# Performance work log

Measured on AMD Instinct MI355X. Metric: run time of the kernel, lower is better.

The kernel has to match this reference:

```python
import jax, jax.numpy as jnp
import numpy as np

B, T, D = 4, 2048, 768
E, F, K = 8, 4 * 768, 2


def setup_inputs() -> dict:
    key = jax.random.key(0)
    ks = jax.random.split(key, 5)
    s = 0.02
    return {
        "x": jax.random.normal(ks[0], (B, T, D), dtype=jnp.float32),
        "Wg": jax.random.normal(ks[1], (D, E), dtype=jnp.float32) * s,
        "bg": jnp.zeros((E,), dtype=jnp.float32),
        "W1": jax.random.normal(ks[2], (E, D, F), dtype=jnp.float32) * s,
        "b1": jnp.zeros((E, F), dtype=jnp.float32),
        "W2": jax.random.normal(ks[3], (E, F, D), dtype=jnp.float32) * s,
        "b2": jnp.zeros((E, D), dtype=jnp.float32),
    }


def reference(x, Wg, bg, W1, b1, W2, b2):
    b, t, d = x.shape
    x_flat = x.reshape(-1, d)                      # [N, D]
    n = x_flat.shape[0]

    # Router: softmax over expert logits, take top-2
    gates = jax.nn.softmax(x_flat @ Wg + bg, axis=-1)   # [N, E]
    topk_g, topk_i = jax.lax.top_k(gates, K)            # [N, K]

    # Combine weights: zero for non-selected experts -> math identical to
    # masked dispatch in the torch loop (out = sum_k gate_k * expert_{idx_k}(x))
    combine = jnp.zeros((n, W1.shape[0]), dtype=gates.dtype)
    combine = combine.at[jnp.arange(n)[:, None], topk_i].add(topk_g)  # [N, E]

    # Per-expert MLP applied densely, then weighted combine (zero weights
    # kill non-selected experts' contributions)
    h = jnp.einsum('nd,edf->enf', x_flat, W1) + b1[:, None, :]  # [E, N, F]
    h = jax.nn.gelu(h, approximate=False)                        # torch nn.GELU = exact
    y = jnp.einsum('enf,efd->end', h, W2) + b2[:, None, :]       # [E, N, D]
    out = jnp.einsum('ne,end->nd', combine, y)                   # [N, D]
    return out.reshape(b, t, d)
```

## Files before the change

### kernel.cpp

```cpp
#include <hip/hip_runtime.h>
#include <hip/hip_bf16.h>


#define N_TOK 8192
#define D_DIM 768
#define E_EXP 8
#define F_DIM 3072
#define CAP   8192
#define NT_MAX 136

typedef __attribute__((ext_vector_type(8))) short s8v;
typedef __attribute__((ext_vector_type(4))) float f4v;
typedef unsigned short u16;
typedef unsigned int   u32;
typedef unsigned long long u64;

static __device__ __forceinline__ u16 f2bf(float f) {
    u32 u = __float_as_uint(f);
    return (u16)((u + 0x7fffu + ((u >> 16) & 1u)) >> 16);
}
static __device__ __forceinline__ float bf2f(u16 v) {
    return __uint_as_float((u32)v << 16);
}
static __device__ __forceinline__ u32 cvt_pk_bf16(float lo, float hi) {
    u32 r;
    asm("v_cvt_pk_bf16_f32 %0, %1, %2" : "=v"(r) : "v"(lo), "v"(hi));
    return r;
}
static __device__ __forceinline__ float gelu_fast(float v) {
    const float av = fabsf(v);
    const float z  = av * 0.70710678118654752440f;
    const float t  = __builtin_amdgcn_rcpf(fmaf(0.3275911f, z, 1.0f));
    const float w  = __builtin_amdgcn_exp2f(-z * z * 1.4426950408889634f);
    float p = fmaf(1.061405429f, t, -1.453152027f);
    p = fmaf(p, t,  1.421413741f);
    p = fmaf(p, t, -0.284496736f);
    p = fmaf(p, t,  0.254829592f);
    p = p * t;
    const float E = 1.0f - p * w;
    return 0.5f * (v + av * E);
}
static __device__ __forceinline__ void gld_lds16(const u16* g, u16* l) {
    __builtin_amdgcn_global_load_lds(
        (const __attribute__((address_space(1))) void*)g,
        (__attribute__((address_space(3))) void*)l, 16, 0, 0);
}
template<int N> static __device__ __forceinline__ void wait_vmcnt() {
    asm volatile("s_waitcnt vmcnt(%0)" :: "n"(N) : "memory");
}
static __device__ __forceinline__ void bar_fenced() {
    asm volatile("s_barrier" ::: "memory");
}

__device__ __forceinline__ void pack_w_body(
    const float* __restrict__ src, u16* __restrict__ dst,
    int rt, int kc64, int e, int K1, int M2, int KC2, int TR, int ntm)
{
    __shared__ float ls[64][132];
    const float* se = src + (size_t)e * K1 * M2;
    const int tid = threadIdx.x;

    const int kr = tid >> 2, mq = tid & 3;
    const float* srow = se + (size_t)(kc64 * 64 + kr) * M2 + rt * 128 + mq * 32;
    #pragma unroll
    for (int it = 0; it < 8; ++it)
        *(float4*)&ls[kr][mq * 32 + it * 4] = *(const float4*)(srow + it * 4);
    __syncthreads();

    u16* dt_ = dst + ((size_t)(e * ntm + (rt * 128) / TR) * KC2 + kc64 * 2)
                     * ((size_t)TR * 32)
                   + (size_t)((rt * 128) % TR) * 32;
    const int rr = tid >> 1, hf = tid & 1;
    u16* dc = dt_ + (size_t)hf * TR * 32;
    const int row = ((rt * 128) % TR) + rr;
    #pragma unroll
    for (int j = 0; j < 4; ++j) {
        union { s8v v; u16 u[8]; } o;
        #pragma unroll
        for (int jj = 0; jj < 8; ++jj)
            o.u[jj] = f2bf(ls[hf * 32 + j * 8 + jj][rr]);
        *(s8v*)&dc[(size_t)rr * 32 + ((j ^ ((row >> 1) & 3)) * 8)] = o.v;
    }
}

__global__ __launch_bounds__(256) void prep_kernel(
    const float* __restrict__ x, const float* __restrict__ Wg,
    const float* __restrict__ bg, const float* __restrict__ W1,
    const float* __restrict__ W2, u32* __restrict__ rec_idx,
    float2* __restrict__ rec_g, u16* __restrict__ w1g,
    u16* __restrict__ w2g, int* __restrict__ counts)
{
    const int bid = blockIdx.x;
    if (bid == 0 && threadIdx.x < E_EXP) counts[threadIdx.x] = 0;

    if (bid < 2048) {
        const int wave = threadIdx.x >> 6;
        const int lane = threadIdx.x & 63;
        const int t = bid * 4 + wave;

        float acc[8];
        #pragma unroll
        for (int e = 0; e < 8; ++e) acc[e] = 0.f;

        const float* xrow = x + (size_t)t * D_DIM + lane * 12;
        #pragma unroll
        for (int i = 0; i < 3; ++i) {
            float4 xv = *(const float4*)(xrow + i * 4);
            float xs[4] = {xv.x, xv.y, xv.z, xv.w};
            #pragma unroll
            for (int j = 0; j < 4; ++j) {
                const int d = lane * 12 + i * 4 + j;
                const float4 w0 = *(const float4*)(Wg + (size_t)d * 8);
                const float4 w1 = *(const float4*)(Wg + (size_t)d * 8 + 4);
                acc[0] += xs[j] * w0.x;  acc[1] += xs[j] * w0.y;
                acc[2] += xs[j] * w0.z;  acc[3] += xs[j] * w0.w;
                acc[4] += xs[j] * w1.x;  acc[5] += xs[j] * w1.y;
                acc[6] += xs[j] * w1.z;  acc[7] += xs[j] * w1.w;
            }
        }
        #pragma unroll
        for (int e = 0; e < 8; ++e) {
            float v = acc[e];
            #pragma unroll
            for (int off = 32; off > 0; off >>= 1) v += __shfl_xor(v, off, 64);
            acc[e] = v + bg[e];
        }
        if (lane == 0) {
            float mx = acc[0];
            #pragma unroll
            for (int e = 1; e < 8; ++e) mx = fmaxf(mx, acc[e]);
            float p[8], s = 0.f;
            #pragma unroll
            for (int e = 0; e < 8; ++e) { p[e] = expf(acc[e] - mx); s += p[e]; }
            const float inv = 1.f / s;
            #pragma unroll
            for (int e = 0; e < 8; ++e) p[e] *= inv;

            int i0 = 0; float g0 = p[0];
            #pragma unroll
            for (int e = 1; e < 8; ++e) if (p[e] > g0) { g0 = p[e]; i0 = e; }
            int i1 = -1; float g1 = -1.f;
            #pragma unroll
            for (int e = 0; e < 8; ++e) if (e != i0 && p[e] > g1) { g1 = p[e]; i1 = e; }

            rec_idx[t] = (u32)i0 | ((u32)i1 << 4);
            rec_g[t] = make_float2(g0, g1);
        }
    } else if (bid < 4352) {
        const int id = bid - 2048;
        const int e = id / 288, rem = id - e * 288;
        const int rt = rem / 12, kc = rem - rt * 12;
        pack_w_body(W1, w1g, rt, kc, e, D_DIM, F_DIM, 24, 256, 12);
    } else {
        const int id = bid - 4352;
        const int e = id / 288, rem = id - e * 288;
        const int rt = rem / 48, kc = rem - rt * 48;
        pack_w_body(W2, w2g, rt, kc, e, F_DIM, D_DIM, 96, 256, 3);
    }
}

__global__ __launch_bounds__(256) void moe_scatter(
    const u32* __restrict__ rec_idx, const float2* __restrict__ rec_g,
    int* __restrict__ counts, int* __restrict__ tokbuf,
    float* __restrict__ gatebuf)
{
    const int t = blockIdx.x * 256 + threadIdx.x;
    const int lane = threadIdx.x & 63;
    const u32 pk = rec_idx[t];
    const int i0 = pk & 15, i1 = (pk >> 4) & 15;
    const float2 g = rec_g[t];
    const u64 lmask = ((u64)1 << lane) - 1;

    #pragma unroll
    for (int e = 0; e < 8; ++e) {
        const u64 m0 = __ballot(i0 == e);
        const u64 m1 = __ballot(i1 == e);
        const int c0 = __popcll(m0);
        const int total = c0 + __popcll(m1);
        if (total > 0) {
            int base = 0;
            if (lane == 0) base = atomicAdd(&counts[e], total);
            base = __shfl(base, 0, 64);
            if (i0 == e) {
                const int p = base + __popcll(m0 & lmask);
                tokbuf[(size_t)e * CAP + p] = 2 * t;
                gatebuf[(size_t)e * CAP + p] = g.x;
            }
            if (i1 == e) {
                const int p = base + c0 + __popcll(m1 & lmask);
                tokbuf[(size_t)e * CAP + p] = 2 * t + 1;
                gatebuf[(size_t)e * CAP + p] = g.y;
            }
        }
    }
}

__global__ void scan_kernel(const int* __restrict__ counts,
                            int* __restrict__ te, int* __restrict__ tb,
                            int* __restrict__ ntile) {
    if (threadIdx.x == 0) {
        int nt = 0;
        for (int e = 0; e < E_EXP; ++e)
            for (int k = 0; k * 128 < counts[e]; ++k) {
                te[nt] = e; tb[nt] = k * 128; ++nt;
            }
        *ntile = nt;
    }
}

__global__ __launch_bounds__(256) void pack_x(
    const float* __restrict__ x, const int* __restrict__ counts,
    const int* __restrict__ te, const int* __restrict__ tb,
    const int* __restrict__ ntile, const int* __restrict__ tokbuf,
    u16* __restrict__ xg)
{
    const int bx = blockIdx.x, kc = blockIdx.y;
    if (bx >= *ntile) return;
    const int e = te[bx], base = tb[bx], cnt = counts[e];
    const int tid = threadIdx.x;
    const int r = tid >> 1, hf = tid & 1;
    int ent = base + r; if (ent >= cnt) ent = cnt - 1;
    const int tok = tokbuf[(size_t)e * CAP + ent] >> 1;
    const float* xr = x + (size_t)tok * D_DIM + kc * 64 + hf * 32;
    u16* xt = xg + ((size_t)bx * 24 + kc * 2 + hf) * 4096;
    #pragma unroll
    for (int j = 0; j < 4; ++j) {
        float4 a = *(const float4*)(xr + j * 8);
        float4 b = *(const float4*)(xr + j * 8 + 4);
        union { s8v v; u16 u[8]; } o;
        o.u[0] = f2bf(a.x); o.u[1] = f2bf(a.y); o.u[2] = f2bf(a.z); o.u[3] = f2bf(a.w);
        o.u[4] = f2bf(b.x); o.u[5] = f2bf(b.y); o.u[6] = f2bf(b.z); o.u[7] = f2bf(b.w);
        *(s8v*)&xt[(size_t)r * 32 + ((j ^ ((r >> 1) & 3)) * 8)] = o.v;
    }
}

#define G_STAGE(S, SBUF) do {                                                 \
    const int S__ = (S) < NS_ ? (S) : NS_ - 1;                                \
    const u16* An_ = Ab + (size_t)S__ * 8192 + w * 2048 + lane * 8;           \
    const u16* Bn_ = Bb + (size_t)S__ * 4096 + w * 1024 + lane * 8;           \
    u16* Ad_ = &Als[SBUF][w * 2048];                                          \
    u16* Bd_ = &Bls[SBUF][w * 1024];                                          \
    gld_lds16(An_,        Ad_);                                               \
    gld_lds16(An_ +  512, Ad_ +  512);                                        \
    gld_lds16(An_ + 1024, Ad_ + 1024);                                        \
    gld_lds16(An_ + 1536, Ad_ + 1536);                                        \
    gld_lds16(Bn_,        Bd_);                                               \
    gld_lds16(Bn_ +  512, Bd_ +  512);                                        \
} while (0)

#define G_STEP(S, BUF, B2) do {                                               \
    wait_vmcnt<6>();                                                          \
    bar_fenced();                                                             \
    G_STAGE((S) + 2, B2);                                                     \
    s8v af[8], bf[4];                                                         \
    _Pragma("unroll")                                                         \
    for (int mi = 0; mi < 8; ++mi)                                            \
        af[mi] = *(const s8v*)&Als[BUF][(wm*128 + mi*16 + ln)*32 + colU];     \
    _Pragma("unroll")                                                         \
    for (int ni = 0; ni < 4; ++ni)                                            \
        bf[ni] = *(const s8v*)&Bls[BUF][(wn*64 + ni*16 + ln)*32 + colU];      \
    __builtin_amdgcn_s_setprio(1);                                            \
    _Pragma("unroll")                                                         \
    for (int mi = 0; mi < 8; ++mi)                                            \
        _Pragma("unroll")                                                     \
        for (int ni = 0; ni < 4; ++ni)                                        \
            acc[mi][ni] = __builtin_amdgcn_mfma_f32_16x16x32_bf16(            \
                af[mi], bf[ni], acc[mi][ni], 0, 0, 0);                        \
    __builtin_amdgcn_s_setprio(0);                                            \
} while (0)

__global__ __launch_bounds__(256, 2) void s1_gemm(
    const u16* __restrict__ xg, const u16* __restrict__ w1g,
    const float* __restrict__ b1, const int* __restrict__ te,
    const int* __restrict__ ntile, u16* __restrict__ hg)
{
    __shared__ __align__(16) u16 Als[3][8192];
    __shared__ __align__(16) u16 Bls[3][4096];
    const int bx = blockIdx.x, by = blockIdx.y;
    if (bx >= *ntile) return;
    const int e = te[bx];
    const int NS_ = 24;

    const int tid  = threadIdx.x;
    const int w    = tid >> 6;
    const int lane = tid & 63;
    const int wm   = w & 1, wn = w >> 1;
    const int q    = lane >> 4, ln = lane & 15;
    const int colU = (q ^ ((ln >> 1) & 3)) * 8;

    const u16* Ab = w1g + (size_t)(e * 12 + by) * 24 * 8192;
    const u16* Bb = xg  + (size_t)bx * 24 * 4096;

    f4v acc[8][4];
    #pragma unroll
    for (int mi = 0; mi < 8; ++mi)
        #pragma unroll
        for (int ni = 0; ni < 4; ++ni) acc[mi][ni] = (f4v){0.f,0.f,0.f,0.f};

    G_STAGE(0, 0);
    G_STAGE(1, 1);

    #pragma unroll 1
    for (int k = 0; k < 24; k += 3) {
        G_STEP(k,     0, 2);
        G_STEP(k + 1, 1, 0);
        G_STEP(k + 2, 2, 1);
    }
    wait_vmcnt<0>();

    const float* b1e = b1 + (size_t)e * F_DIM + by * 256;
    #pragma unroll
    for (int mi = 0; mi < 8; ++mi) {
        const int floc = wm * 128 + mi * 16 + q * 4;
        const int kc2  = by * 8 + (floc >> 5);
        const int cg   = (floc >> 3) & 3;
        const float4 bv = *(const float4*)&b1e[floc];
        #pragma unroll
        for (int ni = 0; ni < 4; ++ni) {
            const int rr = wn * 64 + ni * 16 + ln;
            uint2 pk;
            pk.x = cvt_pk_bf16(gelu_fast(acc[mi][ni][0] + bv.x),
                               gelu_fast(acc[mi][ni][1] + bv.y));
            pk.y = cvt_pk_bf16(gelu_fast(acc[mi][ni][2] + bv.z),
                               gelu_fast(acc[mi][ni][3] + bv.w));
            *(uint2*)&hg[((size_t)bx * 96 + kc2) * 4096 +
                         (size_t)rr * 32 + ((cg ^ ((rr >> 1) & 3)) * 8) +
                         (q & 1) * 4] = pk;
        }
    }
}

__global__ __launch_bounds__(256, 2) void s2_gemm(
    const u16* __restrict__ hg, const u16* __restrict__ w2g,
    const int* __restrict__ counts, const int* __restrict__ te,
    const int* __restrict__ tb, const int* __restrict__ ntile,
    const int* __restrict__ tokbuf, const float* __restrict__ gatebuf,
    u16* __restrict__ y)
{
    __shared__ __align__(16) u16 Als[3][8192];
    __shared__ __align__(16) u16 Bls[3][4096];
    __shared__ int   sts[128];
    __shared__ float sg[128];
    const int bx = blockIdx.x, by = blockIdx.y;
    if (bx >= *ntile) return;
    const int e = te[bx], base = tb[bx], cnt = counts[e];
    const int NS_ = 96;

    const int tid  = threadIdx.x;
    const int w    = tid >> 6;
    const int lane = tid & 63;
    const int wm   = w & 1, wn = w >> 1;
    const int q    = lane >> 4, ln = lane & 15;
    const int colU = (q ^ ((ln >> 1) & 3)) * 8;

    if (tid < 128) {
        const int ent = base + tid;
        const bool v = ent < cnt;
        sts[tid] = v ? tokbuf[(size_t)e * CAP + ent] : -1;
        sg[tid]  = v ? gatebuf[(size_t)e * CAP + ent] : 0.f;
    }
    asm volatile("s_waitcnt vmcnt(0) lgkmcnt(0)" ::: "memory");
    bar_fenced();

    const u16* Ab = w2g + (size_t)(e * 3 + by) * 96 * 8192;
    const u16* Bb = hg  + (size_t)bx * 96 * 4096;

    f4v acc[8][4];
    #pragma unroll
    for (int mi = 0; mi < 8; ++mi)
        #pragma unroll
        for (int ni = 0; ni < 4; ++ni) acc[mi][ni] = (f4v){0.f,0.f,0.f,0.f};

    G_STAGE(0, 0);
    G_STAGE(1, 1);

    #pragma unroll 1
    for (int k = 0; k < 96; k += 3) {
        G_STEP(k,     0, 2);
        G_STEP(k + 1, 1, 0);
        G_STEP(k + 2, 2, 1);
    }
    wait_vmcnt<0>();

    #pragma unroll
    for (int ni = 0; ni < 4; ++ni) {
        const int rr = wn * 64 + ni * 16 + ln;
        const int ts = sts[rr];
        if (ts >= 0) {
            const float g = sg[rr];
            u16* yr = y + (size_t)ts * D_DIM + by * 256 + wm * 128 + q * 4;
            #pragma unroll
            for (int mi = 0; mi < 8; ++mi) {
                uint2 pk;
                pk.x = cvt_pk_bf16(g * acc[mi][ni][0], g * acc[mi][ni][1]);
                pk.y = cvt_pk_bf16(g * acc[mi][ni][2], g * acc[mi][ni][3]);
                *(uint2*)&yr[mi * 16] = pk;
            }
        }
    }
}

__global__ __launch_bounds__(256) void combine_kernel(
    const u16* __restrict__ y, const u32* __restrict__ rec_idx,
    const float2* __restrict__ rec_g, const float* __restrict__ b2,
    float* __restrict__ out)
{
    const int gid = blockIdx.x * 256 + threadIdx.x;
    const int t = gid / 192;
    const int c = (gid - t * 192) * 4;
    const u32 pk = rec_idx[t];
    const int i0 = pk & 15, i1 = (pk >> 4) & 15;
    const float2 g = rec_g[t];
    union { uint2 p; u16 u[4]; } a, b;
    a.p = *(const uint2*)&y[(size_t)(2 * t) * D_DIM + c];
    b.p = *(const uint2*)&y[(size_t)(2 * t + 1) * D_DIM + c];
    const float4 ba = *(const float4*)&b2[(size_t)i0 * D_DIM + c];
    const float4 bb = *(const float4*)&b2[(size_t)i1 * D_DIM + c];
    float4 o;
    o.x = g.x * ba.x + g.y * bb.x + bf2f(a.u[0]) + bf2f(b.u[0]);
    o.y = g.x * ba.y + g.y * bb.y + bf2f(a.u[1]) + bf2f(b.u[1]);
    o.z = g.x * ba.z + g.y * bb.z + bf2f(a.u[2]) + bf2f(b.u[2]);
    o.w = g.x * ba.w + g.y * bb.w + bf2f(a.u[3]) + bf2f(b.u[3]);
    *(float4*)&out[(size_t)t * D_DIM + c] = o;
}

extern "C" void kernel_launch(void* const* d_in, const int* in_sizes, int n_in,
                              void* d_out, int out_size, void* d_ws, size_t ws_size,
                              hipStream_t stream) {
    const float* x  = (const float*)d_in[0];
    const float* Wg = (const float*)d_in[1];
    const float* bg = (const float*)d_in[2];
    const float* W1 = (const float*)d_in[3];
    const float* b1 = (const float*)d_in[4];
    const float* W2 = (const float*)d_in[5];
    const float* b2 = (const float*)d_in[6];
    float* out = (float*)d_out;

    char* ws = (char*)d_ws;
    size_t off = 0;
    u16* xg  = (u16*)(ws + off); off += (size_t)NT_MAX * 24 * 4096 * sizeof(u16);
    u16* w1g = (u16*)(ws + off); off += (size_t)E_EXP * F_DIM * D_DIM * sizeof(u16);
    u16* w2g = (u16*)(ws + off); off += (size_t)E_EXP * D_DIM * F_DIM * sizeof(u16);
    u16* hg  = (u16*)(ws + off); off += (size_t)NT_MAX * 96 * 4096 * sizeof(u16);
    u16* y   = (u16*)(ws + off); off += (size_t)2 * N_TOK * D_DIM * sizeof(u16);
    int* tokbuf = (int*)(ws + off);      off += (size_t)E_EXP * CAP * sizeof(int);
    float* gatebuf = (float*)(ws + off); off += (size_t)E_EXP * CAP * sizeof(float);
    u32* rec_idx = (u32*)(ws + off);     off += (size_t)N_TOK * sizeof(u32);
    float2* rec_g = (float2*)(ws + off); off += (size_t)N_TOK * sizeof(float2);
    int* counts = (int*)(ws + off);      off += 64;
    int* te     = (int*)(ws + off);      off += NT_MAX * sizeof(int);
    int* tb     = (int*)(ws + off);      off += NT_MAX * sizeof(int);
    int* ntile  = (int*)(ws + off);      off += 64;

    prep_kernel<<<6656, 256, 0, stream>>>(x, Wg, bg, W1, W2, rec_idx, rec_g,
                                          w1g, w2g, counts);
    moe_scatter<<<N_TOK / 256, 256, 0, stream>>>(rec_idx, rec_g, counts, tokbuf, gatebuf);
    scan_kernel<<<1, 64, 0, stream>>>(counts, te, tb, ntile);
    pack_x<<<dim3(NT_MAX, 12), 256, 0, stream>>>(x, counts, te, tb, ntile, tokbuf, xg);

    s1_gemm<<<dim3(NT_MAX, 12), 256, 0, stream>>>(xg, w1g, b1, te, ntile, hg);
    s2_gemm<<<dim3(NT_MAX, 3), 256, 0, stream>>>(hg, w2g, counts, te, tb, ntile,
                                                 tokbuf, gatebuf, y);
    combine_kernel<<<(N_TOK * 192) / 256, 256, 0, stream>>>(y, rec_idx, rec_g, b2, out);
}
```

Before: 511.1 us.

## Enlarge expert GEMM token tiles to 256 and switch to 32x32x16 MFMA

Doubles the token tile per expert from 128 to 256 rows in both expert GEMMs and pack_x. Each wave now computes a 128x128 sub-tile with 32x32x16 bf16 MFMA instructions instead of 16x16x32, which raises arithmetic intensity per LDS read and per weight load. The cost is more LDS per block and fewer resident blocks (launch bounds drop to 1 block per SM). Padding waste also grows for experts whose token counts are not multiples of 256, and the grid shrinks, which may under-fill the GPU.

```diff
diff --git a/kernel.cpp b/kernel.cpp
--- a/kernel.cpp
+++ b/kernel.cpp
@@ -7,10 +7,10 @@
 #define E_EXP 8
 #define F_DIM 3072
 #define CAP   8192
-#define NT_MAX 136
-
-typedef __attribute__((ext_vector_type(8))) short s8v;
-typedef __attribute__((ext_vector_type(4))) float f4v;
+#define NT2_MAX 72
+
+typedef __attribute__((ext_vector_type(8)))  short s8v;
+typedef __attribute__((ext_vector_type(16))) float f16v;
 typedef unsigned short u16;
 typedef unsigned int   u32;
 typedef unsigned long long u64;
@@ -201,8 +201,8 @@
     if (threadIdx.x == 0) {
         int nt = 0;
         for (int e = 0; e < E_EXP; ++e)
-            for (int k = 0; k * 128 < counts[e]; ++k) {
-                te[nt] = e; tb[nt] = k * 128; ++nt;
+            for (int k = 0; k * 256 < counts[e]; ++k) {
+                te[nt] = e; tb[nt] = k * 256; ++nt;
             }
         *ntile = nt;
     }
@@ -214,15 +214,17 @@
     const int* __restrict__ ntile, const int* __restrict__ tokbuf,
     u16* __restrict__ xg)
 {
-    const int bx = blockIdx.x, kc = blockIdx.y;
+    const int bx2 = blockIdx.x, kc = blockIdx.y;
+    const int bx = bx2 >> 1, rh = bx2 & 1;
     if (bx >= *ntile) return;
     const int e = te[bx], base = tb[bx], cnt = counts[e];
     const int tid = threadIdx.x;
     const int r = tid >> 1, hf = tid & 1;
-    int ent = base + r; if (ent >= cnt) ent = cnt - 1;
+    const int R = rh * 128 + r;
+    int ent = base + R; if (ent >= cnt) ent = cnt - 1;
     const int tok = tokbuf[(size_t)e * CAP + ent] >> 1;
     const float* xr = x + (size_t)tok * D_DIM + kc * 64 + hf * 32;
-    u16* xt = xg + ((size_t)bx * 24 + kc * 2 + hf) * 4096;
+    u16* xt = xg + ((size_t)bx * 24 + kc * 2 + hf) * 8192;
     #pragma unroll
     for (int j = 0; j < 4; ++j) {
         float4 a = *(const float4*)(xr + j * 8);
@@ -230,52 +232,58 @@
         union { s8v v; u16 u[8]; } o;
         o.u[0] = f2bf(a.x); o.u[1] = f2bf(a.y); o.u[2] = f2bf(a.z); o.u[3] = f2bf(a.w);
         o.u[4] = f2bf(b.x); o.u[5] = f2bf(b.y); o.u[6] = f2bf(b.z); o.u[7] = f2bf(b.w);
-        *(s8v*)&xt[(size_t)r * 32 + ((j ^ ((r >> 1) & 3)) * 8)] = o.v;
+        *(s8v*)&xt[(size_t)R * 32 + ((j ^ ((R >> 1) & 3)) * 8)] = o.v;
     }
 }
 
 #define G_STAGE(S, SBUF) do {                                                 \
     const int S__ = (S) < NS_ ? (S) : NS_ - 1;                                \
     const u16* An_ = Ab + (size_t)S__ * 8192 + w * 2048 + lane * 8;           \
-    const u16* Bn_ = Bb + (size_t)S__ * 4096 + w * 1024 + lane * 8;           \
+    const u16* Bn_ = Bb + (size_t)S__ * 8192 + w * 2048 + lane * 8;           \
     u16* Ad_ = &Als[SBUF][w * 2048];                                          \
-    u16* Bd_ = &Bls[SBUF][w * 1024];                                          \
+    u16* Bd_ = &Bls[SBUF][w * 2048];                                          \
     gld_lds16(An_,        Ad_);                                               \
     gld_lds16(An_ +  512, Ad_ +  512);                                        \
     gld_lds16(An_ + 1024, Ad_ + 1024);                                        \
     gld_lds16(An_ + 1536, Ad_ + 1536);                                        \
     gld_lds16(Bn_,        Bd_);                                               \
     gld_lds16(Bn_ +  512, Bd_ +  512);                                        \
+    gld_lds16(Bn_ + 1024, Bd_ + 1024);                                        \
+    gld_lds16(Bn_ + 1536, Bd_ + 1536);                                        \
 } while (0)
 
 #define G_STEP(S, BUF, B2) do {                                               \
-    wait_vmcnt<6>();                                                          \
+    wait_vmcnt<8>();                                                          \
     bar_fenced();                                                             \
     G_STAGE((S) + 2, B2);                                                     \
-    s8v af[8], bf[4];                                                         \
     _Pragma("unroll")                                                         \
-    for (int mi = 0; mi < 8; ++mi)                                            \
-        af[mi] = *(const s8v*)&Als[BUF][(wm*128 + mi*16 + ln)*32 + colU];     \
-    _Pragma("unroll")                                                         \
-    for (int ni = 0; ni < 4; ++ni)                                            \
-        bf[ni] = *(const s8v*)&Bls[BUF][(wn*64 + ni*16 + ln)*32 + colU];      \
-    __builtin_amdgcn_s_setprio(1);                                            \
-    _Pragma("unroll")                                                         \
-    for (int mi = 0; mi < 8; ++mi)                                            \
+    for (int kk = 0; kk < 2; ++kk) {                                          \
+        const int cswz = ((kk * 2 + hi) ^ ((r32 >> 1) & 3)) * 8;              \
+        s8v af[4], bf[4];                                                     \
         _Pragma("unroll")                                                     \
-        for (int ni = 0; ni < 4; ++ni)                                        \
-            acc[mi][ni] = __builtin_amdgcn_mfma_f32_16x16x32_bf16(            \
-                af[mi], bf[ni], acc[mi][ni], 0, 0, 0);                        \
-    __builtin_amdgcn_s_setprio(0);                                            \
+        for (int mt = 0; mt < 4; ++mt)                                        \
+            af[mt] = *(const s8v*)&Als[BUF][(wm*128 + mt*32 + r32)*32 + cswz];\
+        _Pragma("unroll")                                                     \
+        for (int nt = 0; nt < 4; ++nt)                                        \
+            bf[nt] = *(const s8v*)&Bls[BUF][(wn*128 + nt*32 + r32)*32 + cswz];\
+        __builtin_amdgcn_s_setprio(1);                                        \
+        _Pragma("unroll")                                                     \
+        for (int mt = 0; mt < 4; ++mt)                                        \
+            _Pragma("unroll")                                                 \
+            for (int nt = 0; nt < 4; ++nt)                                    \
+                acc[mt][nt] = __builtin_amdgcn_mfma_f32_32x32x16_bf16(        \
+                    af[mt], bf[nt], acc[mt][nt], 0, 0, 0);                    \
+        __builtin_amdgcn_s_setprio(0);                                        \
+    }                                                                         \
 } while (0)
 
-__global__ __launch_bounds__(256, 2) void s1_gemm(
+__global__ __launch_bounds__(256, 1) void s1_gemm(
     const u16* __restrict__ xg, const u16* __restrict__ w1g,
     const float* __restrict__ b1, const int* __restrict__ te,
     const int* __restrict__ ntile, u16* __restrict__ hg)
 {
     __shared__ __align__(16) u16 Als[3][8192];
-    __shared__ __align__(16) u16 Bls[3][4096];
+    __shared__ __align__(16) u16 Bls[3][8192];
     const int bx = blockIdx.x, by = blockIdx.y;
     if (bx >= *ntile) return;
     const int e = te[bx];
@@ -285,17 +293,18 @@
     const int w    = tid >> 6;
     const int lane = tid & 63;
     const int wm   = w & 1, wn = w >> 1;
-    const int q    = lane >> 4, ln = lane & 15;
-    const int colU = (q ^ ((ln >> 1) & 3)) * 8;
+    const int r32  = lane & 31, hi = lane >> 5;
 
     const u16* Ab = w1g + (size_t)(e * 12 + by) * 24 * 8192;
-    const u16* Bb = xg  + (size_t)bx * 24 * 4096;
-
-    f4v acc[8][4];
-    #pragma unroll
-    for (int mi = 0; mi < 8; ++mi)
-        #pragma unroll
-        for (int ni = 0; ni < 4; ++ni) acc[mi][ni] = (f4v){0.f,0.f,0.f,0.f};
+    const u16* Bb = xg  + (size_t)bx * 24 * 8192;
+
+    f16v acc[4][4];
+    #pragma unroll
+    for (int mt = 0; mt < 4; ++mt)
+        #pragma unroll
+        for (int nt = 0; nt < 4; ++nt)
+            #pragma unroll
+            for (int ee = 0; ee < 16; ++ee) acc[mt][nt][ee] = 0.f;
 
     G_STAGE(0, 0);
     G_STAGE(1, 1);
@@ -310,27 +319,30 @@
 
     const float* b1e = b1 + (size_t)e * F_DIM + by * 256;
     #pragma unroll
-    for (int mi = 0; mi < 8; ++mi) {
-        const int floc = wm * 128 + mi * 16 + q * 4;
-        const int kc2  = by * 8 + (floc >> 5);
-        const int cg   = (floc >> 3) & 3;
-        const float4 bv = *(const float4*)&b1e[floc];
-        #pragma unroll
-        for (int ni = 0; ni < 4; ++ni) {
-            const int rr = wn * 64 + ni * 16 + ln;
-            uint2 pk;
-            pk.x = cvt_pk_bf16(gelu_fast(acc[mi][ni][0] + bv.x),
-                               gelu_fast(acc[mi][ni][1] + bv.y));
-            pk.y = cvt_pk_bf16(gelu_fast(acc[mi][ni][2] + bv.z),
-                               gelu_fast(acc[mi][ni][3] + bv.w));
-            *(uint2*)&hg[((size_t)bx * 96 + kc2) * 4096 +
-                         (size_t)rr * 32 + ((cg ^ ((rr >> 1) & 3)) * 8) +
-                         (q & 1) * 4] = pk;
-        }
-    }
-}
-
-__global__ __launch_bounds__(256, 2) void s2_gemm(
+    for (int mt = 0; mt < 4; ++mt) {
+        const int kc2 = by * 8 + wm * 4 + mt;
+        u16* hc = hg + ((size_t)bx * 96 + kc2) * 8192;
+        #pragma unroll
+        for (int rq = 0; rq < 4; ++rq) {
+            const int floc = wm * 128 + mt * 32 + rq * 8 + hi * 4;
+            const float4 bv = *(const float4*)&b1e[floc];
+            #pragma unroll
+            for (int nt = 0; nt < 4; ++nt) {
+                const int rr = wn * 128 + nt * 32 + r32;
+                const int e0 = rq * 4;
+                uint2 pk;
+                pk.x = cvt_pk_bf16(gelu_fast(acc[mt][nt][e0]     + bv.x),
+                                   gelu_fast(acc[mt][nt][e0 + 1] + bv.y));
+                pk.y = cvt_pk_bf16(gelu_fast(acc[mt][nt][e0 + 2] + bv.z),
+                                   gelu_fast(acc[mt][nt][e0 + 3] + bv.w));
+                *(uint2*)&hc[(size_t)rr * 32 +
+                             ((rq ^ ((rr >> 1) & 3)) * 8) + hi * 4] = pk;
+            }
+        }
+    }
+}
+
+__global__ __launch_bounds__(256, 1) void s2_gemm(
     const u16* __restrict__ hg, const u16* __restrict__ w2g,
     const int* __restrict__ counts, const int* __restrict__ te,
     const int* __restrict__ tb, const int* __restrict__ ntile,
@@ -338,9 +350,9 @@
     u16* __restrict__ y)
 {
     __shared__ __align__(16) u16 Als[3][8192];
-    __shared__ __align__(16) u16 Bls[3][4096];
-    __shared__ int   sts[128];
-    __shared__ float sg[128];
+    __shared__ __align__(16) u16 Bls[3][8192];
+    __shared__ int   sts[256];
+    __shared__ float sg[256];
     const int bx = blockIdx.x, by = blockIdx.y;
     if (bx >= *ntile) return;
     const int e = te[bx], base = tb[bx], cnt = counts[e];
@@ -350,10 +362,9 @@
     const int w    = tid >> 6;
     const int lane = tid & 63;
     const int wm   = w & 1, wn = w >> 1;
-    const int q    = lane >> 4, ln = lane & 15;
-    const int colU = (q ^ ((ln >> 1) & 3)) * 8;
-
-    if (tid < 128) {
+    const int r32  = lane & 31, hi = lane >> 5;
+
+    {
         const int ent = base + tid;
         const bool v = ent < cnt;
         sts[tid] = v ? tokbuf[(size_t)e * CAP + ent] : -1;
@@ -363,13 +374,15 @@
     bar_fenced();
 
     const u16* Ab = w2g + (size_t)(e * 3 + by) * 96 * 8192;
-    const u16* Bb = hg  + (size_t)bx * 96 * 4096;
-
-    f4v acc[8][4];
-    #pragma unroll
-    for (int mi = 0; mi < 8; ++mi)
-        #pragma unroll
-        for (int ni = 0; ni < 4; ++ni) acc[mi][ni] = (f4v){0.f,0.f,0.f,0.f};
+    const u16* Bb = hg  + (size_t)bx * 96 * 8192;
+
+    f16v acc[4][4];
+    #pragma unroll
+    for (int mt = 0; mt < 4; ++mt)
+        #pragma unroll
+        for (int nt = 0; nt < 4; ++nt)
+            #pragma unroll
+            for (int ee = 0; ee < 16; ++ee) acc[mt][nt][ee] = 0.f;
 
     G_STAGE(0, 0);
     G_STAGE(1, 1);
@@ -383,19 +396,24 @@
     wait_vmcnt<0>();
 
     #pragma unroll
-    for (int ni = 0; ni < 4; ++ni) {
-        const int rr = wn * 64 + ni * 16 + ln;
+    for (int nt = 0; nt < 4; ++nt) {
+        const int rr = wn * 128 + nt * 32 + r32;
         const int ts = sts[rr];
         if (ts >= 0) {
             const float g = sg[rr];
-            u16* yr = y + (size_t)ts * D_DIM + by * 256 + wm * 128 + q * 4;
-            #pragma unroll
-            for (int mi = 0; mi < 8; ++mi) {
-                uint2 pk;
-                pk.x = cvt_pk_bf16(g * acc[mi][ni][0], g * acc[mi][ni][1]);
-                pk.y = cvt_pk_bf16(g * acc[mi][ni][2], g * acc[mi][ni][3]);
-                *(uint2*)&yr[mi * 16] = pk;
-            }
+            u16* yr = y + (size_t)ts * D_DIM + by * 256 + wm * 128 + hi * 4;
+            #pragma unroll
+            for (int mt = 0; mt < 4; ++mt)
+                #pragma unroll
+                for (int rq = 0; rq < 4; ++rq) {
+                    const int e0 = rq * 4;
+                    uint2 pk;
+                    pk.x = cvt_pk_bf16(g * acc[mt][nt][e0],
+                                       g * acc[mt][nt][e0 + 1]);
+                    pk.y = cvt_pk_bf16(g * acc[mt][nt][e0 + 2],
+                                       g * acc[mt][nt][e0 + 3]);
+                    *(uint2*)&yr[mt * 32 + rq * 8] = pk;
+                }
         }
     }
 }
@@ -438,28 +456,29 @@
 
     char* ws = (char*)d_ws;
     size_t off = 0;
-    u16* xg  = (u16*)(ws + off); off += (size_t)NT_MAX * 24 * 4096 * sizeof(u16);
+    u16* xg  = (u16*)(ws + off); off += (size_t)NT2_MAX * 24 * 8192 * sizeof(u16);
     u16* w1g = (u16*)(ws + off); off += (size_t)E_EXP * F_DIM * D_DIM * sizeof(u16);
     u16* w2g = (u16*)(ws + off); off += (size_t)E_EXP * D_DIM * F_DIM * sizeof(u16);
-    u16* hg  = (u16*)(ws + off); off += (size_t)NT_MAX * 96 * 4096 * sizeof(u16);
+    u16* hg  = (u16*)(ws + off); off += (size_t)NT2_MAX * 96 * 8192 * sizeof(u16);
     u16* y   = (u16*)(ws + off); off += (size_t)2 * N_TOK * D_DIM * sizeof(u16);
     int* tokbuf = (int*)(ws + off);      off += (size_t)E_EXP * CAP * sizeof(int);
     float* gatebuf = (float*)(ws + off); off += (size_t)E_EXP * CAP * sizeof(float);
     u32* rec_idx = (u32*)(ws + off);     off += (size_t)N_TOK * sizeof(u32);
     float2* rec_g = (float2*)(ws + off); off += (size_t)N_TOK * sizeof(float2);
     int* counts = (int*)(ws + off);      off += 64;
-    int* te     = (int*)(ws + off);      off += NT_MAX * sizeof(int);
-    int* tb     = (int*)(ws + off);      off += NT_MAX * sizeof(int);
+    int* te     = (int*)(ws + off);      off += NT2_MAX * sizeof(int);
+    int* tb     = (int*)(ws + off);      off += NT2_MAX * sizeof(int);
     int* ntile  = (int*)(ws + off);      off += 64;
 
     prep_kernel<<<6656, 256, 0, stream>>>(x, Wg, bg, W1, W2, rec_idx, rec_g,
                                           w1g, w2g, counts);
     moe_scatter<<<N_TOK / 256, 256, 0, stream>>>(rec_idx, rec_g, counts, tokbuf, gatebuf);
     scan_kernel<<<1, 64, 0, stream>>>(counts, te, tb, ntile);
-    pack_x<<<dim3(NT_MAX, 12), 256, 0, stream>>>(x, counts, te, tb, ntile, tokbuf, xg);
-
-    s1_gemm<<<dim3(NT_MAX, 12), 256, 0, stream>>>(xg, w1g, b1, te, ntile, hg);
-    s2_gemm<<<dim3(NT_MAX, 3), 256, 0, stream>>>(hg, w2g, counts, te, tb, ntile,
-                                                 tokbuf, gatebuf, y);
+    pack_x<<<dim3(NT2_MAX * 2, 12), 256, 0, stream>>>(x, counts, te, tb, ntile,
+                                                      tokbuf, xg);
+
+    s1_gemm<<<dim3(NT2_MAX, 12), 256, 0, stream>>>(xg, w1g, b1, te, ntile, hg);
+    s2_gemm<<<dim3(NT2_MAX, 3), 256, 0, stream>>>(hg, w2g, counts, te, tb, ntile,
+                                                  tokbuf, gatebuf, y);
     combine_kernel<<<(N_TOK * 192) / 256, 256, 0, stream>>>(y, rec_idx, rec_g, b2, out);
 }
```

After: 624.0 us. 22.1% more time.

## Split GEMM k-step into two half-phases interleaving LDS reads, async loads and MFMA

Applied to the files above, without the earlier changes.

Each k-step of the shared GEMM mainloop now runs as two halves. Each half loads four A fragments from LDS, issues half of the next stage's global-to-LDS loads, synchronises, and runs 16 MFMAs, instead of one big load-then-compute block. The wait for the next buffer moves to the end of the step, and a prologue wait is added. The aim is finer interleaving of memory traffic with matrix ops and fewer live fragment registers, at the cost of extra barriers per step.

```diff
diff --git a/kernel.cpp b/kernel.cpp
--- a/kernel.cpp
+++ b/kernel.cpp
@@ -47,6 +47,10 @@
 }
 template<int N> static __device__ __forceinline__ void wait_vmcnt() {
     asm volatile("s_waitcnt vmcnt(%0)" :: "n"(N) : "memory");
+}
+static __device__ __forceinline__ void wait_lgkm0() {
+    asm volatile("s_waitcnt lgkmcnt(0)" ::: "memory");
+    __builtin_amdgcn_sched_barrier(0);
 }
 static __device__ __forceinline__ void bar_fenced() {
     asm volatile("s_barrier" ::: "memory");
@@ -248,25 +252,60 @@
     gld_lds16(Bn_ +  512, Bd_ +  512);                                        \
 } while (0)
 
+#define G_STAGE_H0(S, SBUF) do {                                              \
+    const int S__ = (S) < NS_ ? (S) : NS_ - 1;                                \
+    const u16* An_ = Ab + (size_t)S__ * 8192 + w * 2048 + lane * 8;           \
+    const u16* Bn_ = Bb + (size_t)S__ * 4096 + w * 1024 + lane * 8;           \
+    gld_lds16(An_,       &Als[SBUF][w * 2048]);                               \
+    gld_lds16(An_ + 512, &Als[SBUF][w * 2048 + 512]);                         \
+    gld_lds16(Bn_,       &Bls[SBUF][w * 1024]);                               \
+} while (0)
+
+#define G_STAGE_H1(S, SBUF) do {                                              \
+    const int S__ = (S) < NS_ ? (S) : NS_ - 1;                                \
+    const u16* An_ = Ab + (size_t)S__ * 8192 + w * 2048 + lane * 8;           \
+    const u16* Bn_ = Bb + (size_t)S__ * 4096 + w * 1024 + lane * 8;           \
+    gld_lds16(An_ + 1024, &Als[SBUF][w * 2048 + 1024]);                       \
+    gld_lds16(An_ + 1536, &Als[SBUF][w * 2048 + 1536]);                       \
+    gld_lds16(Bn_ + 512,  &Bls[SBUF][w * 1024 + 512]);                        \
+} while (0)
+
 #define G_STEP(S, BUF, B2) do {                                               \
-    wait_vmcnt<6>();                                                          \
-    bar_fenced();                                                             \
-    G_STAGE((S) + 2, B2);                                                     \
-    s8v af[8], bf[4];                                                         \
+    s8v af[4], bf[4];                                                         \
     _Pragma("unroll")                                                         \
-    for (int mi = 0; mi < 8; ++mi)                                            \
+    for (int mi = 0; mi < 4; ++mi)                                            \
         af[mi] = *(const s8v*)&Als[BUF][(wm*128 + mi*16 + ln)*32 + colU];     \
     _Pragma("unroll")                                                         \
     for (int ni = 0; ni < 4; ++ni)                                            \
         bf[ni] = *(const s8v*)&Bls[BUF][(wn*64 + ni*16 + ln)*32 + colU];      \
+    G_STAGE_H0((S) + 2, B2);                                                  \
+    bar_fenced();                                                             \
+    wait_lgkm0();                                                             \
     __builtin_amdgcn_s_setprio(1);                                            \
     _Pragma("unroll")                                                         \
-    for (int mi = 0; mi < 8; ++mi)                                            \
+    for (int mi = 0; mi < 4; ++mi)                                            \
         _Pragma("unroll")                                                     \
         for (int ni = 0; ni < 4; ++ni)                                        \
             acc[mi][ni] = __builtin_amdgcn_mfma_f32_16x16x32_bf16(            \
                 af[mi], bf[ni], acc[mi][ni], 0, 0, 0);                        \
     __builtin_amdgcn_s_setprio(0);                                            \
+    bar_fenced();                                                             \
+    _Pragma("unroll")                                                         \
+    for (int mi = 0; mi < 4; ++mi)                                            \
+        af[mi] = *(const s8v*)&Als[BUF][(wm*128 + (mi+4)*16 + ln)*32 + colU]; \
+    G_STAGE_H1((S) + 2, B2);                                                  \
+    bar_fenced();                                                             \
+    wait_lgkm0();                                                             \
+    __builtin_amdgcn_s_setprio(1);                                            \
+    _Pragma("unroll")                                                         \
+    for (int mi = 0; mi < 4; ++mi)                                            \
+        _Pragma("unroll")                                                     \
+        for (int ni = 0; ni < 4; ++ni)                                        \
+            acc[4 + mi][ni] = __builtin_amdgcn_mfma_f32_16x16x32_bf16(        \
+                af[mi], bf[ni], acc[4 + mi][ni], 0, 0, 0);                    \
+    __builtin_amdgcn_s_setprio(0);                                            \
+    wait_vmcnt<6>();                                                          \
+    bar_fenced();                                                             \
 } while (0)
 
 __global__ __launch_bounds__(256, 2) void s1_gemm(
@@ -299,6 +338,8 @@
 
     G_STAGE(0, 0);
     G_STAGE(1, 1);
+    wait_vmcnt<6>();
+    bar_fenced();
 
     #pragma unroll 1
     for (int k = 0; k < 24; k += 3) {
@@ -373,6 +414,8 @@
 
     G_STAGE(0, 0);
     G_STAGE(1, 1);
+    wait_vmcnt<6>();
+    bar_fenced();
 
     #pragma unroll 1
     for (int k = 0; k < 96; k += 3) {
```

New measurement: 526.1 us. +2.9%, slower.
